# Kernel optimization log

Hardware: AMD Instinct MI355X
Metric: run time of the kernel (lower is better)

Reference implementation:

```python
import jax, jax.numpy as jnp
import numpy as np

N_BONDS = 50000
N_EDGES = 600000
BOND_DIM = 64
SPH_DIM = 64
UNITS = 64


def setup_inputs() -> dict:
    key = jax.random.key(0)
    k1, k2, k3, k4, k5 = jax.random.split(key, 5)
    bond_features = jax.random.normal(k1, (N_BONDS, BOND_DIM), dtype=jnp.float32)
    edges_sph_features = jax.random.normal(k2, (N_EDGES, SPH_DIM), dtype=jnp.float32)
    # column 0: sorted segment ids (tf.math.segment_sum requires sorted ids)
    seg = jnp.sort(jax.random.randint(k3, (N_EDGES,), 0, N_BONDS, dtype=jnp.int32))
    nbr = jax.random.randint(k4, (N_EDGES,), 0, N_BONDS, dtype=jnp.int32)
    edges_neighbor = jnp.stack([seg, nbr], axis=1)  # [n_edges, 2]
    kernel = jax.random.normal(k5, (BOND_DIM + SPH_DIM, UNITS), dtype=jnp.float32) * 0.05
    bias = jnp.zeros((UNITS,), dtype=jnp.float32)
    return {
        "bond_features": bond_features,
        "edges_sph_features": edges_sph_features,
        "edges_neighbor": edges_neighbor,
        "kernel": kernel,
        "bias": bias,
    }


def reference(bond_features, edges_sph_features, edges_neighbor, kernel, bias):
    # gather bond features of the neighboring bond for each edge (line-graph)
    gathered = bond_features[edges_neighbor[:, 1]]            # [E, bond_dim]
    concated = jnp.concatenate([gathered, edges_sph_features], axis=-1)  # [E, bond_dim+sph_dim]
    # scatter-reduce into segments (sorted ids; fixed num_segments for jit)
    aggregated = jax.ops.segment_sum(
        concated, edges_neighbor[:, 0], num_segments=N_BONDS,
        indices_are_sorted=True,
    )  # [n_bonds, bond_dim+sph_dim]
    return aggregated @ kernel + bias
```

## Files before the change

kernel.cpp:

```cpp
#include <hip/hip_runtime.h>

#define N_BONDS 50000
#define N_EDGES 600000
#define R_BONDS 8
#define BONDS_PER_BLOCK 32

typedef float f4 __attribute__((ext_vector_type(4)));

__device__ __forceinline__ float bcastf(float v, int l) {
    return __builtin_bit_cast(float, __builtin_amdgcn_readlane(__builtin_bit_cast(int, v), l));
}
__device__ __forceinline__ f4 f4zero() { return (f4){0.f, 0.f, 0.f, 0.f}; }
__device__ __forceinline__ void fma4(f4& a, float s, const f4& b) {
    a.x = fmaf(s, b.x, a.x); a.y = fmaf(s, b.y, a.y);
    a.z = fmaf(s, b.z, a.z); a.w = fmaf(s, b.w, a.w);
}

__global__ __launch_bounds__(256)
void fill_starts(const int* __restrict__ edges, int* __restrict__ starts) {
    const int e = blockIdx.x * blockDim.x + threadIdx.x;
    if (e >= N_EDGES) return;
    const int2* edges2 = (const int2*)edges;
    const int s  = edges2[e].x;
    const int sp = (e == 0) ? -1 : edges2[e - 1].x;
    for (int b = sp + 1; b <= s; ++b) starts[b] = e;
    if (e == N_EDGES - 1)
        for (int b = s + 1; b <= N_BONDS; ++b) starts[b] = N_EDGES;
}

__global__ __launch_bounds__(256, 4)
void fused_gather_segsum_mm(const float* __restrict__ bond,
                            const float* __restrict__ sph,
                            const int*   __restrict__ edges,
                            const float* __restrict__ Kmat,
                            const float* __restrict__ bias,
                            const int*   __restrict__ starts,
                            float* __restrict__ out)
{
    __shared__ float ldsK[128 * 64];
    const int tid  = threadIdx.x;
    const int lane = tid & 63;
    const int wid  = tid >> 6;
    const int fl   = lane & 15;
    const int sg   = lane >> 4;

    {
        const f4* K4 = (const f4*)Kmat;
        f4*       L4 = (f4*)ldsK;
        #pragma unroll
        for (int i = 0; i < 8; ++i) L4[tid + i * 256] = K4[tid + i * 256];
    }
    __syncthreads();

    const int b0 = blockIdx.x * BONDS_PER_BLOCK + wid * R_BONDS;
    if (b0 >= N_BONDS) return;

    int st[R_BONDS + 1];
    #pragma unroll
    for (int r = 0; r <= R_BONDS; ++r)
        st[r] = __builtin_amdgcn_readfirstlane(starts[b0 + r]);

    const int eb    = st[0];
    const int total = st[R_BONDS] - eb;

    const f4*   bond4  = (const f4*)bond;
    const f4*   sph4   = (const f4*)sph;
    const int2* edges2 = (const int2*)edges;

    float slotG[R_BONDS], slotS[R_BONDS];
    f4 aG = f4zero(), aS = f4zero();
    int r = 0, cs = 0, bnd = st[1] - eb;

    auto txr = [&](f4 v) -> float {
        v.x += __shfl_xor(v.x, 16); v.y += __shfl_xor(v.y, 16);
        v.z += __shfl_xor(v.z, 16); v.w += __shfl_xor(v.w, 16);
        v.x += __shfl_xor(v.x, 32); v.y += __shfl_xor(v.y, 32);
        v.z += __shfl_xor(v.z, 32); v.w += __shfl_xor(v.w, 32);
        const int src = lane >> 2;
        const float s0 = __shfl(v.x, src), s1 = __shfl(v.y, src);
        const float s2 = __shfl(v.z, src), s3 = __shfl(v.w, src);
        const float r01 = (lane & 1) ? s1 : s0;
        const float r23 = (lane & 1) ? s3 : s2;
        return (lane & 2) ? r23 : r01;
    };

    auto slowpath = [&](int q, f4 GV, f4 SV) {
        const int qe = q + sg;
        while (true) {
            const float m = (qe >= cs && qe < bnd) ? 1.f : 0.f;
            fma4(aG, m, GV); fma4(aS, m, SV);
            if (bnd > q + 4) break;
            const float tG = txr(aG), tS = txr(aS);
            #pragma unroll
            for (int rr = 0; rr < R_BONDS; ++rr)
                if (rr == r) { slotG[rr] = tG; slotS[rr] = tS; }
            aG = f4zero(); aS = f4zero();
            cs = bnd;
            ++r;
            if (r >= R_BONDS) { bnd = 0x7fffffff; break; }
            #pragma unroll
            for (int rr = 2; rr <= R_BONDS; ++rr)
                if (r + 1 == rr) bnd = st[rr] - eb;
        }
    };

    int w0 = 0;
    while (w0 < total) {
        int wlen = total - w0; if (wlen > 64) wlen = 64;
        int2 p = make_int2(0, 0);
        if (lane < wlen) p = edges2[eb + w0 + lane];
        const int ng = (wlen + 3) >> 2;

        for (int c = 0; c < ng; c += 4) {
            f4 g0, g1, g2, g3, s0, s1, s2, s3;

#define ISSUE(GG, GV, SV) do { \
            if ((c + GG) < ng) { \
                const int idx_ = (c + GG) * 4 + sg; \
                const int nbr_ = __shfl(p.y, idx_); \
                int qe_ = w0 + idx_; if (qe_ >= total) qe_ = total - 1; \
                GV = bond4[nbr_ * 16 + fl]; \
                SV = __builtin_nontemporal_load(&sph4[(eb + qe_) * 16 + fl]); \
            } else { GV = f4zero(); SV = f4zero(); } } while (0)

            ISSUE(0, g0, s0); ISSUE(1, g1, s1); ISSUE(2, g2, s2); ISSUE(3, g3, s3);
#undef ISSUE

#define ACCG(GG, GV, SV) do { \
            if ((c + GG) < ng) { \
                const int q_ = w0 + (c + GG) * 4; \
                if (q_ + 4 <= bnd) { aG += GV; aS += SV; } \
                else slowpath(q_, GV, SV); \
            } } while (0)

            ACCG(0, g0, s0); ACCG(1, g1, s1); ACCG(2, g2, s2); ACCG(3, g3, s3);
#undef ACCG
        }
        w0 += wlen;
    }

    {
        const float tG = txr(aG), tS = txr(aS);
        #pragma unroll
        for (int rr = 0; rr < R_BONDS; ++rr) {
            if (rr == r)     { slotG[rr] = tG;  slotS[rr] = tS; }
            else if (rr > r) { slotG[rr] = 0.f; slotS[rr] = 0.f; }
        }
    }

    float acc[R_BONDS];
    const float bl = bias[lane];
    #pragma unroll
    for (int rr = 0; rr < R_BONDS; ++rr) acc[rr] = bl;

    #pragma unroll 2
    for (int d = 0; d < 64; ++d) {
        const float kt = ldsK[d * 64 + lane];
        const float kb = ldsK[(64 + d) * 64 + lane];
        #pragma unroll
        for (int rr = 0; rr < R_BONDS; ++rr) {
            acc[rr] = fmaf(bcastf(slotG[rr], d), kt, acc[rr]);
            acc[rr] = fmaf(bcastf(slotS[rr], d), kb, acc[rr]);
        }
    }

    #pragma unroll
    for (int rr = 0; rr < R_BONDS; ++rr)
        if (b0 + rr < N_BONDS)
            __builtin_nontemporal_store(acc[rr], &out[(b0 + rr) * 64 + lane]);
}

extern "C" void kernel_launch(void* const* d_in, const int* in_sizes, int n_in,
                              void* d_out, int out_size, void* d_ws, size_t ws_size,
                              hipStream_t stream) {
    const float* bond  = (const float*)d_in[0];
    const float* sph   = (const float*)d_in[1];
    const int*   edges = (const int*)d_in[2];
    const float* Kmat  = (const float*)d_in[3];
    const float* bias  = (const float*)d_in[4];
    float* out  = (float*)d_out;
    int* starts = (int*)d_ws;

    fill_starts<<<(N_EDGES + 255) / 256, 256, 0, stream>>>(edges, starts);

    const int nblocks = (N_BONDS + BONDS_PER_BLOCK - 1) / BONDS_PER_BLOCK;
    fused_gather_segsum_mm<<<nblocks, 256, 0, stream>>>(bond, sph, edges, Kmat,
                                                        bias, starts, out);
}
```

Before: 79.60 us.

## Use 8 waves of 4 bonds per block and software-pipeline the edge gather loop

Each wave now handles 4 bonds instead of 8, and blocks have 512 threads so each block still covers 32 bonds. The gather loop becomes a rolling software pipeline: the next group's bond and sph loads are issued right after the current group is accumulated, so several memory requests stay in flight. The launch-bounds target rises to 8 blocks per CU and the matmul loop unroll goes from 2 to 4. The aim is more memory-level parallelism and occupancy in a gather-bound kernel, at the cost of register pressure and more per-wave setup.

```diff
diff --git a/kernel.cpp b/kernel.cpp
--- a/kernel.cpp
+++ b/kernel.cpp
@@ -2,7 +2,8 @@
 
 #define N_BONDS 50000
 #define N_EDGES 600000
-#define R_BONDS 8
+#define R_BONDS 4
+#define THREADS 512
 #define BONDS_PER_BLOCK 32
 
 typedef float f4 __attribute__((ext_vector_type(4)));
@@ -28,7 +29,7 @@
         for (int b = s + 1; b <= N_BONDS; ++b) starts[b] = N_EDGES;
 }
 
-__global__ __launch_bounds__(256, 4)
+__global__ __launch_bounds__(THREADS, 8)
 void fused_gather_segsum_mm(const float* __restrict__ bond,
                             const float* __restrict__ sph,
                             const int*   __restrict__ edges,
@@ -48,7 +49,7 @@
         const f4* K4 = (const f4*)Kmat;
         f4*       L4 = (f4*)ldsK;
         #pragma unroll
-        for (int i = 0; i < 8; ++i) L4[tid + i * 256] = K4[tid + i * 256];
+        for (int i = 0; i < 4; ++i) L4[tid + i * THREADS] = K4[tid + i * THREADS];
     }
     __syncthreads();
 
@@ -111,31 +112,35 @@
         if (lane < wlen) p = edges2[eb + w0 + lane];
         const int ng = (wlen + 3) >> 2;
 
-        for (int c = 0; c < ng; c += 4) {
-            f4 g0, g1, g2, g3, s0, s1, s2, s3;
+        f4 gA, sA, gB, sB, gC, sC, gD, sD;
 
-#define ISSUE(GG, GV, SV) do { \
-            if ((c + GG) < ng) { \
-                const int idx_ = (c + GG) * 4 + sg; \
-                const int nbr_ = __shfl(p.y, idx_); \
-                int qe_ = w0 + idx_; if (qe_ >= total) qe_ = total - 1; \
-                GV = bond4[nbr_ * 16 + fl]; \
-                SV = __builtin_nontemporal_load(&sph4[(eb + qe_) * 16 + fl]); \
-            } else { GV = f4zero(); SV = f4zero(); } } while (0)
+#define ISS(QQ, GV, SV) do { \
+        if ((QQ) < ng) { \
+            const int idx_ = (QQ) * 4 + sg; \
+            const int nbr_ = __shfl(p.y, idx_); \
+            int qe_ = w0 + idx_; if (qe_ >= total) qe_ = total - 1; \
+            GV = bond4[nbr_ * 16 + fl]; \
+            SV = __builtin_nontemporal_load(&sph4[(eb + qe_) * 16 + fl]); \
+        } else { GV = f4zero(); SV = f4zero(); } } while (0)
 
-            ISSUE(0, g0, s0); ISSUE(1, g1, s1); ISSUE(2, g2, s2); ISSUE(3, g3, s3);
-#undef ISSUE
+#define ACC(QQ, GV, SV) do { \
+        const int q_ = w0 + (QQ) * 4; \
+        if (q_ + 4 <= bnd) { aG += GV; aS += SV; } \
+        else slowpath(q_, GV, SV); } while (0)
 
-#define ACCG(GG, GV, SV) do { \
-            if ((c + GG) < ng) { \
-                const int q_ = w0 + (c + GG) * 4; \
-                if (q_ + 4 <= bnd) { aG += GV; aS += SV; } \
-                else slowpath(q_, GV, SV); \
-            } } while (0)
-
-            ACCG(0, g0, s0); ACCG(1, g1, s1); ACCG(2, g2, s2); ACCG(3, g3, s3);
-#undef ACCG
+        ISS(0, gA, sA); ISS(1, gB, sB); ISS(2, gC, sC); ISS(3, gD, sD);
+        int q = 0;
+        for (; q + 4 <= ng; q += 4) {
+            ACC(q + 0, gA, sA); ISS(q + 4, gA, sA);
+            ACC(q + 1, gB, sB); ISS(q + 5, gB, sB);
+            ACC(q + 2, gC, sC); ISS(q + 6, gC, sC);
+            ACC(q + 3, gD, sD); ISS(q + 7, gD, sD);
         }
+        if (q + 0 < ng) ACC(q + 0, gA, sA);
+        if (q + 1 < ng) ACC(q + 1, gB, sB);
+        if (q + 2 < ng) ACC(q + 2, gC, sC);
+#undef ISS
+#undef ACC
         w0 += wlen;
     }
 
@@ -153,7 +158,7 @@
     #pragma unroll
     for (int rr = 0; rr < R_BONDS; ++rr) acc[rr] = bl;
 
-    #pragma unroll 2
+    #pragma unroll 4
     for (int d = 0; d < 64; ++d) {
         const float kt = ldsK[d * 64 + lane];
         const float kb = ldsK[(64 + d) * 64 + lane];
@@ -184,6 +189,6 @@
     fill_starts<<<(N_EDGES + 255) / 256, 256, 0, stream>>>(edges, starts);
 
     const int nblocks = (N_BONDS + BONDS_PER_BLOCK - 1) / BONDS_PER_BLOCK;
-    fused_gather_segsum_mm<<<nblocks, 256, 0, stream>>>(bond, sph, edges, Kmat,
-                                                        bias, starts, out);
+    fused_gather_segsum_mm<<<nblocks, THREADS, 0, stream>>>(bond, sph, edges, Kmat,
+                                                            bias, starts, out);
 }
```

Result: slower. 103.3 us (+29.8%).
